# Kernel tuning notes

Hardware: AMD Instinct MI355X
Metric: run time of the kernel (lower is better)

Reference implementation:

```python
import jax, jax.numpy as jnp
import numpy as np

N_NODES = 100000
N_EDGES = 1000000
EMB = 64
HID = 64
N_CLASSES = 1
LEAKY_SLOPE = 0.01  # flax.linen.leaky_relu default


def setup_inputs() -> dict:
    key = jax.random.key(0)
    k1, k2, k3, k4, k5 = jax.random.split(key, 5)
    node_ids = jnp.arange(N_NODES, dtype=jnp.int32)
    senders = jax.random.randint(k1, (N_EDGES,), 0, N_NODES, dtype=jnp.int32)
    receivers = jax.random.randint(k2, (N_EDGES,), 0, N_NODES, dtype=jnp.int32)
    embed_table = jax.random.normal(k3, (N_NODES, EMB), dtype=jnp.float32) * 0.05
    W1 = jax.random.normal(k4, (EMB, HID), dtype=jnp.float32) * (1.0 / np.sqrt(EMB))
    W2 = jax.random.normal(k5, (HID, N_CLASSES), dtype=jnp.float32) * (1.0 / np.sqrt(HID))
    b2 = jnp.zeros((N_CLASSES,), dtype=jnp.float32)
    return {"node_ids": node_ids, "senders": senders, "receivers": receivers,
            "embed_table": embed_table, "W1": W1, "W2": W2, "b2": b2}


def gcn_aggregate(x, senders, receivers, n_nodes, symmetric):
    # Faithful to jraph.GraphConvolution: update_node_fn is applied BEFORE this.
    if symmetric:
        ones = jnp.ones_like(senders, dtype=x.dtype)
        send_deg = jax.ops.segment_sum(ones, senders, num_segments=n_nodes)
        recv_deg = jax.ops.segment_sum(ones, receivers, num_segments=n_nodes)
        x = x * jax.lax.rsqrt(jnp.maximum(send_deg, 1.0))[:, None]
        x = jax.ops.segment_sum(x[senders], receivers, num_segments=n_nodes)  # [N, d]
        x = x * jax.lax.rsqrt(jnp.maximum(recv_deg, 1.0))[:, None]
    else:
        x = jax.ops.segment_sum(x[senders], receivers, num_segments=n_nodes)
    return x


def reference(node_ids, senders, receivers, embed_table, W1, W2, b2):
    n = node_ids.shape[0]
    # GraphMapFeatures(embed_node_fn=nn.Embed(...))
    x = embed_table[node_ids]                      # [N, EMB]
    # GraphConvolution(Dense(hidden, use_bias=False), symmetric_normalization=True)
    x = x @ W1                                     # [N, HID]
    x = gcn_aggregate(x, senders, receivers, n, symmetric=True)
    x = jax.nn.leaky_relu(x, negative_slope=LEAKY_SLOPE)
    # GraphConvolution(Dense(classes), symmetric_normalization=False)
    x = x @ W2 + b2                                # [N, C]
    x = gcn_aggregate(x, senders, receivers, n, symmetric=False)
    return jax.nn.sigmoid(x)
```

## Files before the change

kernel.cpp:

```cpp
#include <hip/hip_runtime.h>
#include <hip/hip_bf16.h>

#define N_NODES 100000
#define N_EDGES 1000000
#define SCAN_B 256
#define N_BLOCKS_SCAN ((N_NODES + SCAN_B - 1) / SCAN_B)

#define RANGES 4
#define RSIZE  25000
#define RWORDS 12500
#define CHUNKS 32
#define CHUNK_EDGES (N_EDGES / CHUNKS)
#define HRSIZE  12500
#define HRWORDS 6250


__device__ __forceinline__ unsigned f32_to_bf16(float v) {
    unsigned u = __float_as_uint(v);
    return (u + 0x7fffu + ((u >> 16) & 1u)) >> 16;
}

__global__ void k_hist(const int* __restrict__ senders,
                       const int* __restrict__ receivers,
                       unsigned* __restrict__ ghist_s,
                       unsigned* __restrict__ ghist_r) {
    __shared__ unsigned lds[RWORDS];
    int blk = blockIdx.x;
    int arr = blk >> 7;
    int rem = blk & 127;
    int r   = rem >> 5;
    int c   = rem & 31;
    const int* __restrict__ src = arr ? receivers : senders;
    unsigned* __restrict__ gh   = arr ? ghist_r : ghist_s;
    int t = threadIdx.x;

    for (int w = t; w < RWORDS; w += 1024) lds[w] = 0u;
    __syncthreads();

    int base = r * RSIZE;
    int beg  = c * CHUNK_EDGES;
    int end  = beg + CHUNK_EDGES;
    for (int i = beg + t; i < end; i += 1024) {
        unsigned idx = (unsigned)(src[i] - base);
        if (idx < (unsigned)RSIZE)
            atomicAdd(&lds[idx >> 1], 1u << ((idx & 1) * 16));
    }
    __syncthreads();

    unsigned* __restrict__ dst = gh + (size_t)rem * RWORDS;
    for (int w = t; w < RWORDS; w += 1024) dst[w] = lds[w];
}

__global__ void k_scanA2(const unsigned* __restrict__ ghist_s,
                         const unsigned* __restrict__ ghist_r,
                         int* __restrict__ cnt_r, float* __restrict__ rs,
                         int* __restrict__ blockSums) {
    __shared__ int s[SCAN_B];
    int t = threadIdx.x;
    int idx = blockIdx.x * SCAN_B + t;
    int v = 0;
    if (idx < N_NODES) {
        int r = idx / RSIZE;
        int bin = idx - r * RSIZE;
        int w = bin >> 1, sh = (bin & 1) * 16;
        const unsigned* __restrict__ gr = ghist_r + (size_t)(r * CHUNKS) * RWORDS + w;
        const unsigned* __restrict__ gs = ghist_s + (size_t)(r * CHUNKS) * RWORDS + w;
        unsigned sr_ = 0, ss_ = 0;
#pragma unroll
        for (int c = 0; c < CHUNKS; ++c) {
            sr_ += (gr[(size_t)c * RWORDS] >> sh) & 0xffffu;
            ss_ += (gs[(size_t)c * RWORDS] >> sh) & 0xffffu;
        }
        v = (int)sr_;
        cnt_r[idx] = v;
        rs[idx] = rsqrtf(fmaxf((float)ss_, 1.0f));
    }
    s[t] = v;
    __syncthreads();
    for (int off = 1; off < SCAN_B; off <<= 1) {
        int x = (t >= off) ? s[t - off] : 0;
        __syncthreads();
        s[t] += x;
        __syncthreads();
    }
    if (t == SCAN_B - 1) blockSums[blockIdx.x] = s[t];
}

__global__ void k_scanB(const int* __restrict__ blockSums, int* __restrict__ blockOffs) {
    __shared__ int s[512];
    int t = threadIdx.x;
    int v = (t < N_BLOCKS_SCAN) ? blockSums[t] : 0;
    s[t] = v;
    __syncthreads();
    for (int off = 1; off < 512; off <<= 1) {
        int x = (t >= off) ? s[t - off] : 0;
        __syncthreads();
        s[t] += x;
        __syncthreads();
    }
    if (t < N_BLOCKS_SCAN) blockOffs[t] = s[t] - v;
}

__global__ void k_scanCD(const int* __restrict__ cnt_r,
                         const int* __restrict__ blockOffs,
                         const unsigned* __restrict__ ghist_r,
                         int* __restrict__ row_start,
                         int* __restrict__ coff) {
    __shared__ int s[SCAN_B];
    int t = threadIdx.x;
    int idx = blockIdx.x * SCAN_B + t;
    int v = (idx < N_NODES) ? cnt_r[idx] : 0;
    s[t] = v;
    __syncthreads();
    for (int off = 1; off < SCAN_B; off <<= 1) {
        int x = (t >= off) ? s[t - off] : 0;
        __syncthreads();
        s[t] += x;
        __syncthreads();
    }
    if (idx < N_NODES) {
        int run = blockOffs[blockIdx.x] + s[t] - v;
        row_start[idx] = run;
        int r = idx / RSIZE;
        int bin = idx - r * RSIZE;
        int w = bin >> 1, sh = (bin & 1) * 16;
        const unsigned* __restrict__ gr = ghist_r + (size_t)(r * CHUNKS) * RWORDS + w;
        int* __restrict__ co = coff + (size_t)(r * CHUNKS) * RSIZE + bin;
#pragma unroll
        for (int c = 0; c < CHUNKS; ++c) {
            co[(size_t)c * RSIZE] = run;
            run += (int)((gr[(size_t)c * RWORDS] >> sh) & 0xffffu);
        }
    }
    if (blockIdx.x == 0 && t == 0) row_start[N_NODES] = N_EDGES;
}

__global__ void k_fill2(const int* __restrict__ senders,
                        const int* __restrict__ receivers,
                        const int* __restrict__ coff,
                        int* __restrict__ col) {
    __shared__ unsigned lds[HRWORDS];
    int r8 = blockIdx.x >> 5;
    int c  = blockIdx.x & 31;
    int sr = r8 >> 1, hs = r8 & 1;
    int t  = threadIdx.x;

    for (int w = t; w < HRWORDS; w += 1024) lds[w] = 0u;
    __syncthreads();

    int base = r8 * HRSIZE;
    int beg  = c * CHUNK_EDGES, end = beg + CHUNK_EDGES;
    const int* __restrict__ co =
        coff + (size_t)(sr * CHUNKS + c) * RSIZE + hs * HRSIZE;
    for (int i = beg + t; i < end; i += 1024) {
        unsigned idx = (unsigned)(receivers[i] - base);
        if (idx < (unsigned)HRSIZE) {
            int sh = (idx & 1) * 16;
            unsigned old = atomicAdd(&lds[idx >> 1], 1u << sh);
            int rank = (int)((old >> sh) & 0xffffu);
            col[co[idx] + rank] = senders[i];
        }
    }
}

__global__ void k_h(const float* __restrict__ emb,
                    const float* __restrict__ rs,
                    const float* __restrict__ W1,
                    unsigned short* __restrict__ h16) {
    int lane = threadIdx.x & 63;
    int wib  = threadIdx.x >> 6;
    int wpb  = blockDim.x >> 6;
    int gw   = blockIdx.x * wpb + wib;
    int nw   = gridDim.x * wpb;

    float w1c[64];
#pragma unroll
    for (int k = 0; k < 64; ++k) w1c[k] = W1[k * 64 + lane];

    for (int n = gw; n < N_NODES; n += nw) {
        float e = emb[(size_t)n * 64 + lane] * rs[n];
        float a = 0.f;
        int ei = __float_as_int(e);
#pragma unroll
        for (int k = 0; k < 64; ++k)
            a += __int_as_float(__builtin_amdgcn_readlane(ei, k)) * w1c[k];
        h16[(size_t)n * 64 + lane] = (unsigned short)f32_to_bf16(a);
    }
}

__global__ void k_agg_post(const int* __restrict__ row_start,
                           const int* __restrict__ col,
                           const unsigned* __restrict__ h32,
                           const float* __restrict__ W2,
                           const float* __restrict__ b2,
                           float* __restrict__ z) {
    int gtid = blockIdx.x * blockDim.x + threadIdx.x;
    int wid  = gtid >> 6;
    int lane = threadIdx.x & 63;
    int half = lane >> 5;
    int hl   = lane & 31;
    int n = wid * 2 + half;
    if (n >= N_NODES) return;

    int start = row_start[n];
    int end   = row_start[n + 1];
    float a0 = 0.f, a1 = 0.f;
    int i = start;
    for (; i + 3 < end; i += 4) {
        int s0 = col[i], s1 = col[i + 1], s2 = col[i + 2], s3 = col[i + 3];
        unsigned u0 = h32[(size_t)s0 * 32 + hl];
        unsigned u1 = h32[(size_t)s1 * 32 + hl];
        unsigned u2 = h32[(size_t)s2 * 32 + hl];
        unsigned u3 = h32[(size_t)s3 * 32 + hl];
        a0 += (__uint_as_float(u0 << 16) + __uint_as_float(u1 << 16)) +
              (__uint_as_float(u2 << 16) + __uint_as_float(u3 << 16));
        a1 += (__uint_as_float(u0 & 0xffff0000u) + __uint_as_float(u1 & 0xffff0000u)) +
              (__uint_as_float(u2 & 0xffff0000u) + __uint_as_float(u3 & 0xffff0000u));
    }
    for (; i < end; ++i) {
        unsigned u = h32[(size_t)col[i] * 32 + hl];
        a0 += __uint_as_float(u << 16);
        a1 += __uint_as_float(u & 0xffff0000u);
    }

    float rsq = rsqrtf(fmaxf((float)(end - start), 1.0f));
    float x0 = a0 * rsq, x1 = a1 * rsq;
    x0 = (x0 > 0.f) ? x0 : 0.01f * x0;
    x1 = (x1 > 0.f) ? x1 : 0.01f * x1;
    float2 w2 = ((const float2*)W2)[hl];
    float p = x0 * w2.x + x1 * w2.y;
#pragma unroll
    for (int off = 16; off > 0; off >>= 1) p += __shfl_xor(p, off, 64);
    if (hl == 0) z[n] = p + b2[0];
}

__global__ void k_agg2_sigmoid(const int* __restrict__ row_start,
                               const int* __restrict__ col,
                               const float* __restrict__ z,
                               float* __restrict__ out) {
    int n = blockIdx.x * blockDim.x + threadIdx.x;
    if (n >= N_NODES) return;
    int start = row_start[n];
    int end   = row_start[n + 1];
    float acc = 0.f;
    int i = start;
    for (; i + 3 < end; i += 4) {
        float a = z[col[i]],     b = z[col[i + 1]];
        float c = z[col[i + 2]], d = z[col[i + 3]];
        acc += (a + b) + (c + d);
    }
    for (; i < end; ++i) acc += z[col[i]];
    out[n] = 1.0f / (1.0f + expf(-acc));
}

extern "C" void kernel_launch(void* const* d_in, const int* in_sizes, int n_in,
                              void* d_out, int out_size, void* d_ws, size_t ws_size,
                              hipStream_t stream) {
    const int* senders    = (const int*)d_in[1];
    const int* receivers  = (const int*)d_in[2];
    const float* emb      = (const float*)d_in[3];
    const float* W1       = (const float*)d_in[4];
    const float* W2       = (const float*)d_in[5];
    const float* b2       = (const float*)d_in[6];
    float* out            = (float*)d_out;

    char* ws = (char*)d_ws;
    unsigned*       ghist_s   = (unsigned*)(ws);
    unsigned*       ghist_r   = (unsigned*)(ws + 6400000);
    int*            coff      = (int*)(ws + 12800000);
    int*            cnt_r     = (int*)(ws + 25600000);
    int*            row_start = (int*)(ws + 26000000);
    int*            blockSums = (int*)(ws + 26400016);
    int*            blockOffs = (int*)(ws + 26401600);
    float*          rs        = (float*)(ws + 26403200);
    int*            col       = (int*)(ws + 26803200);
    unsigned short* h16       = (unsigned short*)(ws + 30803200);
    float*          z         = (float*)(ws + 43603200);

    const int B = 256;
    k_hist<<<2 * RANGES * CHUNKS, 1024, 0, stream>>>(senders, receivers, ghist_s, ghist_r);
    k_scanA2<<<N_BLOCKS_SCAN, SCAN_B, 0, stream>>>(ghist_s, ghist_r, cnt_r, rs, blockSums);
    k_scanB<<<1, 512, 0, stream>>>(blockSums, blockOffs);
    k_scanCD<<<N_BLOCKS_SCAN, SCAN_B, 0, stream>>>(cnt_r, blockOffs, ghist_r, row_start, coff);
    k_fill2<<<RANGES * CHUNKS * 2, 1024, 0, stream>>>(senders, receivers, coff, col);
    k_h<<<2048, 256, 0, stream>>>(emb, rs, W1, h16);
    k_agg_post<<<12500, B, 0, stream>>>(row_start, col, (const unsigned*)h16, W2, b2, z);
    k_agg2_sigmoid<<<(N_NODES + B - 1) / B, B, 0, stream>>>(row_start, col, z, out);
}
```

Baseline: 213.6 us.

## Fold block-offset scan into scanCD and co-launch the W1 projection kernel

Removes the single-block scanB launch by having each scan block reduce the preceding blockSums itself. It also merges the k_h projection (emb*rs @ W1 to bf16) into the same launch as extra blocks, so the projection runs alongside the offset computation instead of after k_fill2. This cuts two kernel launches and overlaps independent work. In exchange, each scan block does redundant prefix summation, and the h part now uses 1024 blocks instead of 2048.

```diff
diff --git a/kernel.cpp b/kernel.cpp
--- a/kernel.cpp
+++ b/kernel.cpp
@@ -5,6 +5,7 @@
 #define N_EDGES 1000000
 #define SCAN_B 256
 #define N_BLOCKS_SCAN ((N_NODES + SCAN_B - 1) / SCAN_B)
+#define H_BLOCKS 1024
 
 #define RANGES 4
 #define RSIZE  25000
@@ -86,53 +87,76 @@
     if (t == SCAN_B - 1) blockSums[blockIdx.x] = s[t];
 }
 
-__global__ void k_scanB(const int* __restrict__ blockSums, int* __restrict__ blockOffs) {
-    __shared__ int s[512];
-    int t = threadIdx.x;
-    int v = (t < N_BLOCKS_SCAN) ? blockSums[t] : 0;
-    s[t] = v;
-    __syncthreads();
-    for (int off = 1; off < 512; off <<= 1) {
-        int x = (t >= off) ? s[t - off] : 0;
-        __syncthreads();
-        s[t] += x;
-        __syncthreads();
-    }
-    if (t < N_BLOCKS_SCAN) blockOffs[t] = s[t] - v;
-}
-
-__global__ void k_scanCD(const int* __restrict__ cnt_r,
-                         const int* __restrict__ blockOffs,
-                         const unsigned* __restrict__ ghist_r,
-                         int* __restrict__ row_start,
-                         int* __restrict__ coff) {
+__global__ void k_scanCD_h(const int* __restrict__ cnt_r,
+                           const int* __restrict__ blockSums,
+                           const unsigned* __restrict__ ghist_r,
+                           int* __restrict__ row_start,
+                           int* __restrict__ coff,
+                           const float* __restrict__ emb,
+                           const float* __restrict__ rs,
+                           const float* __restrict__ W1,
+                           unsigned short* __restrict__ h16) {
     __shared__ int s[SCAN_B];
     int t = threadIdx.x;
-    int idx = blockIdx.x * SCAN_B + t;
-    int v = (idx < N_NODES) ? cnt_r[idx] : 0;
-    s[t] = v;
-    __syncthreads();
-    for (int off = 1; off < SCAN_B; off <<= 1) {
-        int x = (t >= off) ? s[t - off] : 0;
-        __syncthreads();
-        s[t] += x;
-        __syncthreads();
-    }
-    if (idx < N_NODES) {
-        int run = blockOffs[blockIdx.x] + s[t] - v;
-        row_start[idx] = run;
-        int r = idx / RSIZE;
-        int bin = idx - r * RSIZE;
-        int w = bin >> 1, sh = (bin & 1) * 16;
-        const unsigned* __restrict__ gr = ghist_r + (size_t)(r * CHUNKS) * RWORDS + w;
-        int* __restrict__ co = coff + (size_t)(r * CHUNKS) * RSIZE + bin;
-#pragma unroll
-        for (int c = 0; c < CHUNKS; ++c) {
-            co[(size_t)c * RSIZE] = run;
-            run += (int)((gr[(size_t)c * RWORDS] >> sh) & 0xffffu);
-        }
-    }
-    if (blockIdx.x == 0 && t == 0) row_start[N_NODES] = N_EDGES;
+    int b = blockIdx.x;
+
+    if (b < N_BLOCKS_SCAN) {
+        int acc = 0;
+        for (int j = t; j < b; j += SCAN_B) acc += blockSums[j];
+        s[t] = acc;
+        __syncthreads();
+        for (int off = SCAN_B / 2; off > 0; off >>= 1) {
+            if (t < off) s[t] += s[t + off];
+            __syncthreads();
+        }
+        int blockOff = s[0];
+        __syncthreads();
+
+        int idx = b * SCAN_B + t;
+        int v = (idx < N_NODES) ? cnt_r[idx] : 0;
+        s[t] = v;
+        __syncthreads();
+        for (int off = 1; off < SCAN_B; off <<= 1) {
+            int x = (t >= off) ? s[t - off] : 0;
+            __syncthreads();
+            s[t] += x;
+            __syncthreads();
+        }
+        if (idx < N_NODES) {
+            int run = blockOff + s[t] - v;
+            row_start[idx] = run;
+            int r = idx / RSIZE;
+            int bin = idx - r * RSIZE;
+            int w = bin >> 1, sh = (bin & 1) * 16;
+            const unsigned* __restrict__ gr = ghist_r + (size_t)(r * CHUNKS) * RWORDS + w;
+            int* __restrict__ co = coff + (size_t)(r * CHUNKS) * RSIZE + bin;
+#pragma unroll
+            for (int c = 0; c < CHUNKS; ++c) {
+                co[(size_t)c * RSIZE] = run;
+                run += (int)((gr[(size_t)c * RWORDS] >> sh) & 0xffffu);
+            }
+        }
+        if (b == 0 && t == 0) row_start[N_NODES] = N_EDGES;
+    } else {
+        int lane = t & 63;
+        int wib  = t >> 6;
+        int gw   = (b - N_BLOCKS_SCAN) * 4 + wib;
+        const int nw = H_BLOCKS * 4;
+
+        float w1c[64];
+#pragma unroll
+        for (int k = 0; k < 64; ++k) w1c[k] = W1[k * 64 + lane];
+
+        for (int n = gw; n < N_NODES; n += nw) {
+            float e = emb[(size_t)n * 64 + lane] * rs[n];
+            float a = 0.f;
+            int ei = __float_as_int(e);
+#pragma unroll
+            for (int k = 0; k < 64; ++k)
+                a += __int_as_float(__builtin_amdgcn_readlane(ei, k)) * w1c[k];
+            h16[(size_t)n * 64 + lane] = (unsigned short)f32_to_bf16(a);
+        }
+    }
 }
 
 __global__ void k_fill2(const int* __restrict__ senders,
@@ -160,31 +184,6 @@
             int rank = (int)((old >> sh) & 0xffffu);
             col[co[idx] + rank] = senders[i];
         }
-    }
-}
-
-__global__ void k_h(const float* __restrict__ emb,
-                    const float* __restrict__ rs,
-                    const float* __restrict__ W1,
-                    unsigned short* __restrict__ h16) {
-    int lane = threadIdx.x & 63;
-    int wib  = threadIdx.x >> 6;
-    int wpb  = blockDim.x >> 6;
-    int gw   = blockIdx.x * wpb + wib;
-    int nw   = gridDim.x * wpb;
-
-    float w1c[64];
-#pragma unroll
-    for (int k = 0; k < 64; ++k) w1c[k] = W1[k * 64 + lane];
-
-    for (int n = gw; n < N_NODES; n += nw) {
-        float e = emb[(size_t)n * 64 + lane] * rs[n];
-        float a = 0.f;
-        int ei = __float_as_int(e);
-#pragma unroll
-        for (int k = 0; k < 64; ++k)
-            a += __int_as_float(__builtin_amdgcn_readlane(ei, k)) * w1c[k];
-        h16[(size_t)n * 64 + lane] = (unsigned short)f32_to_bf16(a);
     }
 }
 
@@ -271,7 +270,6 @@
     int*            cnt_r     = (int*)(ws + 25600000);
     int*            row_start = (int*)(ws + 26000000);
     int*            blockSums = (int*)(ws + 26400016);
-    int*            blockOffs = (int*)(ws + 26401600);
     float*          rs        = (float*)(ws + 26403200);
     int*            col       = (int*)(ws + 26803200);
     unsigned short* h16       = (unsigned short*)(ws + 30803200);
@@ -280,10 +278,9 @@
     const int B = 256;
     k_hist<<<2 * RANGES * CHUNKS, 1024, 0, stream>>>(senders, receivers, ghist_s, ghist_r);
     k_scanA2<<<N_BLOCKS_SCAN, SCAN_B, 0, stream>>>(ghist_s, ghist_r, cnt_r, rs, blockSums);
-    k_scanB<<<1, 512, 0, stream>>>(blockSums, blockOffs);
-    k_scanCD<<<N_BLOCKS_SCAN, SCAN_B, 0, stream>>>(cnt_r, blockOffs, ghist_r, row_start, coff);
+    k_scanCD_h<<<N_BLOCKS_SCAN + H_BLOCKS, B, 0, stream>>>(
+        cnt_r, blockSums, ghist_r, row_start, coff, emb, rs, W1, h16);
     k_fill2<<<RANGES * CHUNKS * 2, 1024, 0, stream>>>(senders, receivers, coff, col);
-    k_h<<<2048, 256, 0, stream>>>(emb, rs, W1, h16);
     k_agg_post<<<12500, B, 0, stream>>>(row_start, col, (const unsigned*)h16, W2, b2, z);
     k_agg2_sigmoid<<<(N_NODES + B - 1) / B, B, 0, stream>>>(row_start, col, z, out);
 }
```

Measured after the change: 212.1 us (median of 2 runs). No clear change (-0.7%).
